# Kernel optimization log

Measured on AMD Instinct MI355X. Metric: run time of the kernel, lower is better.

The kernel has to match this reference:

```python
import jax, jax.numpy as jnp
import numpy as np

B, S, D, R = 8, 512, 768, 128


def setup_inputs() -> dict:
    key = jax.random.key(0)
    k1, k2, k3 = jax.random.split(key, 3)
    embeddings = jax.random.normal(k1, (B, S, D), dtype=jnp.float32)
    # nn.init.uniform_(proj, -0.05, 0.05)
    proj_dist = jax.random.uniform(k2, (R, D), dtype=jnp.float32, minval=-0.05, maxval=0.05)
    proj_depth = jax.random.uniform(k3, (R, D), dtype=jnp.float32, minval=-0.05, maxval=0.05)
    return {"embeddings": embeddings, "proj_dist": proj_dist, "proj_depth": proj_depth}


def _distances(embeddings, proj):
    # (B,S,D) @ (D,R) -> (B,S,R)
    p = jnp.einsum('bsd,rd->bsr', embeddings, proj)
    # pairwise squared euclidean distances: sum_r (p_i - p_j)^2 -> (B,S,S)
    diff = p[:, :, None, :] - p[:, None, :, :]
    return jnp.sum(diff * diff, axis=-1)


def _depths(embeddings, proj):
    p = jnp.einsum('bsd,rd->bsr', embeddings, proj)
    return jnp.sum(p * p, axis=-1)  # (B,S)


def reference(embeddings, proj_dist, proj_depth):
    distances = _distances(embeddings, proj_dist)
    depths = _depths(embeddings, proj_depth)
    return (distances, depths)
```

## Files before the change

### kernel.cpp

```cpp
#include <hip/hip_runtime.h>

#define NB 8
#define NS 512
#define ND 768
#define NR 128
#define NM (NB * NS)
#define DIST_ELEMS ((size_t)NB * NS * NS)

typedef short bf16x8 __attribute__((ext_vector_type(8)));
typedef __bf16 bfv8  __attribute__((ext_vector_type(8)));
typedef float f32x4  __attribute__((ext_vector_type(4)));

__device__ __forceinline__ unsigned short f2bf(float f) {
  return __builtin_bit_cast(unsigned short, (__bf16)f);
}
__device__ __forceinline__ float bf2f(unsigned short h) {
  return __uint_as_float(((unsigned int)h) << 16);
}
__device__ __forceinline__ bf16x8 pack8(float4 lo, float4 hi) {
  bfv8 v;
  v[0] = (__bf16)lo.x; v[1] = (__bf16)lo.y;
  v[2] = (__bf16)lo.z; v[3] = (__bf16)lo.w;
  v[4] = (__bf16)hi.x; v[5] = (__bf16)hi.y;
  v[6] = (__bf16)hi.z; v[7] = (__bf16)hi.w;
  return __builtin_bit_cast(bf16x8, v);
}

constexpr int KT  = 128;
constexpr int SAS = 136;

__global__ __launch_bounds__(256) void proj_kernel(
    const float* __restrict__ emb,
    const float* __restrict__ projD,
    const float* __restrict__ projP,
    unsigned short* __restrict__ P,
    float* __restrict__ nP0, float* __restrict__ nP1,
    float* __restrict__ nD0, float* __restrict__ nD1)
{
  __shared__ unsigned short sA[2][32][SAS];
  __shared__ float sRed[4][32];

  const int tid = threadIdx.x;
  const int m0  = blockIdx.x * 32;
  const int ct  = blockIdx.y;
  const bool isP = (ct < 2);
  const float* proj = (isP ? projD : projP) + (size_t)((ct & 1) * 64) * ND;

  const int ar = tid >> 3, ao = tid & 7;
  const float* aPtr = emb + (size_t)(m0 + ar) * ND + ao * 8;

  const int lane = tid & 63;
  const int w    = tid >> 6;
  const int ln   = lane & 15;
  const int q    = lane >> 4;

  const float* bRow = proj + (size_t)(16 * w + ln) * ND + q * 8;

  float4 a0, a1, a2, a3;
  a0 = *(const float4*)(aPtr);      a1 = *(const float4*)(aPtr + 4);
  a2 = *(const float4*)(aPtr + 64); a3 = *(const float4*)(aPtr + 68);

  f32x4 acc[2] = {};

  *(bf16x8*)(&sA[0][ar][ao * 8])       = pack8(a0, a1);
  *(bf16x8*)(&sA[0][ar][(ao + 8) * 8]) = pack8(a2, a3);
  __syncthreads();

  int p = 0;
  for (int kt = 0; kt < ND; kt += KT) {
    const bool more = (kt + KT < ND);
    if (more) {
      const int o = kt + KT;
      a0 = *(const float4*)(aPtr + o);      a1 = *(const float4*)(aPtr + o + 4);
      a2 = *(const float4*)(aPtr + o + 64); a3 = *(const float4*)(aPtr + o + 68);
    }
    bf16x8 bq[4];
    #pragma unroll
    for (int ks = 0; ks < 4; ++ks) {
      const float* bp = bRow + kt + ks * 32;
      float4 lo = *(const float4*)bp;
      float4 hi = *(const float4*)(bp + 4);
      bq[ks] = pack8(lo, hi);
    }
    #pragma unroll
    for (int ks = 0; ks < 4; ++ks) {
      #pragma unroll
      for (int i = 0; i < 2; ++i) {
        bf16x8 aq = *(const bf16x8*)(&sA[p][16 * i + ln][ks * 32 + q * 8]);
        acc[i] = __builtin_amdgcn_mfma_f32_16x16x32_bf16(aq, bq[ks], acc[i], 0, 0, 0);
      }
    }
    if (more) {
      *(bf16x8*)(&sA[p ^ 1][ar][ao * 8])       = pack8(a0, a1);
      *(bf16x8*)(&sA[p ^ 1][ar][(ao + 8) * 8]) = pack8(a2, a3);
    }
    __syncthreads();
    p ^= 1;
  }

  const int colG = (ct & 1) * 64 + 16 * w + ln;
  #pragma unroll
  for (int i = 0; i < 2; ++i)
    #pragma unroll
    for (int r = 0; r < 4; ++r) {
      unsigned short hb = f2bf(acc[i][r]);
      if (isP) P[(size_t)(m0 + 16 * i + 4 * q + r) * NR + colG] = hb;
      float v = bf2f(hb);
      float s = v * v;
      s += __shfl_xor(s, 1);
      s += __shfl_xor(s, 2);
      s += __shfl_xor(s, 4);
      s += __shfl_xor(s, 8);
      if (ln == 0) sRed[w][16 * i + 4 * q + r] = s;
    }
  __syncthreads();
  if (tid < 32) {
    float* np = (ct == 0) ? nP0 : (ct == 1) ? nP1 : (ct == 2) ? nD0 : nD1;
    np[m0 + tid] = sRed[0][tid] + sRed[1][tid] + sRed[2][tid] + sRed[3][tid];
  }
}

__global__ __launch_bounds__(256) void dist_kernel(
    const unsigned short* __restrict__ P,
    const float* __restrict__ nP0, const float* __restrict__ nP1,
    const float* __restrict__ nD0, const float* __restrict__ nD1,
    float* __restrict__ out,
    float* __restrict__ depths)
{
  __shared__ float nIs[64], nJs[64];

  const int tid = threadIdx.x;
  const int b  = blockIdx.z;
  const int i0 = blockIdx.y * 64;
  const int j0 = blockIdx.x * 64;
  const unsigned short* Pb = P + (size_t)b * NS * NR;
  const int mB = b * NS;

  if (tid < 64) {
    nIs[tid] = nP0[mB + i0 + tid] + nP1[mB + i0 + tid];
  } else if (tid < 128) {
    const int t = tid - 64;
    nJs[t] = nP0[mB + j0 + t] + nP1[mB + j0 + t];
  } else if (blockIdx.x == 0 && tid < 192) {
    const int t = tid - 128;
    depths[mB + i0 + t] = nD0[mB + i0 + t] + nD1[mB + i0 + t];
  }

  const int lane = tid & 63;
  const int w    = tid >> 6;
  const int ln   = lane & 15;
  const int q    = lane >> 4;

  bf16x8 aq[4][4], bq[4];
  #pragma unroll
  for (int ks = 0; ks < 4; ++ks) {
    bq[ks] = *(const bf16x8*)(Pb + (size_t)(j0 + 16 * w + ln) * NR + ks * 32 + q * 8);
    #pragma unroll
    for (int i = 0; i < 4; ++i)
      aq[i][ks] = *(const bf16x8*)(Pb + (size_t)(i0 + 16 * i + ln) * NR + ks * 32 + q * 8);
  }

  f32x4 acc[4] = {};
  #pragma unroll
  for (int ks = 0; ks < 4; ++ks)
    #pragma unroll
    for (int i = 0; i < 4; ++i)
      acc[i] = __builtin_amdgcn_mfma_f32_16x16x32_bf16(aq[i][ks], bq[ks], acc[i], 0, 0, 0);

  __syncthreads();

  const int col = j0 + 16 * w + ln;
  const float nj = nJs[16 * w + ln];
  float* ob = out + (size_t)b * NS * NS;
  #pragma unroll
  for (int i = 0; i < 4; ++i)
    #pragma unroll
    for (int r = 0; r < 4; ++r) {
      const int rloc = 16 * i + 4 * q + r;
      ob[(size_t)(i0 + rloc) * NS + col] = nIs[rloc] + nj - 2.0f * acc[i][r];
    }
}

extern "C" void kernel_launch(void* const* d_in, const int* in_sizes, int n_in,
                              void* d_out, int out_size, void* d_ws, size_t ws_size,
                              hipStream_t stream) {
  const float* emb   = (const float*)d_in[0];
  const float* projD = (const float*)d_in[1];
  const float* projP = (const float*)d_in[2];
  float* out = (float*)d_out;

  unsigned short* P = (unsigned short*)d_ws;
  float* nP0 = (float*)((char*)d_ws + (size_t)NM * NR * 2);
  float* nP1 = nP0 + NM;
  float* nD0 = nP1 + NM;
  float* nD1 = nD0 + NM;
  float* depths = out + DIST_ELEMS;

  proj_kernel<<<dim3(NM / 32, 4), 256, 0, stream>>>(emb, projD, projP, P, nP0, nP1, nD0, nD1);
  dist_kernel<<<dim3(NS / 64, NS / 64, NB), 256, 0, stream>>>(P, nP0, nP1, nD0, nD1, out, depths);
}
```

Baseline: 85.48 us.

## Register-prefetch next K-tile of A and B in proj kernel with single barrier

```diff
diff --git a/kernel.cpp b/kernel.cpp
--- a/kernel.cpp
+++ b/kernel.cpp
@@ -27,6 +27,7 @@
 }
 
 constexpr int KT  = 128;
+constexpr int NKT = ND / KT;
 constexpr int SAS = 136;
 
 __global__ __launch_bounds__(256) void proj_kernel(
@@ -56,46 +57,52 @@
 
   const float* bRow = proj + (size_t)(16 * w + ln) * ND + q * 8;
 
-  float4 a0, a1, a2, a3;
-  a0 = *(const float4*)(aPtr);      a1 = *(const float4*)(aPtr + 4);
-  a2 = *(const float4*)(aPtr + 64); a3 = *(const float4*)(aPtr + 68);
+  float4 Ar[2][4], Br[2][8];
+  Ar[0][0] = *(const float4*)(aPtr);      Ar[0][1] = *(const float4*)(aPtr + 4);
+  Ar[0][2] = *(const float4*)(aPtr + 64); Ar[0][3] = *(const float4*)(aPtr + 68);
+  Br[0][0] = *(const float4*)(bRow);      Br[0][1] = *(const float4*)(bRow + 4);
+  Br[0][2] = *(const float4*)(bRow + 32); Br[0][3] = *(const float4*)(bRow + 36);
+  Br[0][4] = *(const float4*)(bRow + 64); Br[0][5] = *(const float4*)(bRow + 68);
+  Br[0][6] = *(const float4*)(bRow + 96); Br[0][7] = *(const float4*)(bRow + 100);
 
   f32x4 acc[2] = {};
 
-  *(bf16x8*)(&sA[0][ar][ao * 8])       = pack8(a0, a1);
-  *(bf16x8*)(&sA[0][ar][(ao + 8) * 8]) = pack8(a2, a3);
-  __syncthreads();
-
-  int p = 0;
-  for (int kt = 0; kt < ND; kt += KT) {
-    const bool more = (kt + KT < ND);
-    if (more) {
-      const int o = kt + KT;
-      a0 = *(const float4*)(aPtr + o);      a1 = *(const float4*)(aPtr + o + 4);
-      a2 = *(const float4*)(aPtr + o + 64); a3 = *(const float4*)(aPtr + o + 68);
+  #pragma unroll
+  for (int t = 0; t < NKT; ++t) {
+    const int cur = t & 1;
+    *(bf16x8*)(&sA[cur][ar][ao * 8])       = pack8(Ar[cur][0], Ar[cur][1]);
+    *(bf16x8*)(&sA[cur][ar][(ao + 8) * 8]) = pack8(Ar[cur][2], Ar[cur][3]);
+    asm volatile("s_waitcnt lgkmcnt(0)" ::: "memory");
+    __builtin_amdgcn_s_barrier();
+    __builtin_amdgcn_sched_barrier(0);
+    if (t + 1 < NKT) {
+      const int o = (t + 1) * KT;
+      const int nxt = cur ^ 1;
+      Ar[nxt][0] = *(const float4*)(aPtr + o);
+      Ar[nxt][1] = *(const float4*)(aPtr + o + 4);
+      Ar[nxt][2] = *(const float4*)(aPtr + o + 64);
+      Ar[nxt][3] = *(const float4*)(aPtr + o + 68);
+      Br[nxt][0] = *(const float4*)(bRow + o);
+      Br[nxt][1] = *(const float4*)(bRow + o + 4);
+      Br[nxt][2] = *(const float4*)(bRow + o + 32);
+      Br[nxt][3] = *(const float4*)(bRow + o + 36);
+      Br[nxt][4] = *(const float4*)(bRow + o + 64);
+      Br[nxt][5] = *(const float4*)(bRow + o + 68);
+      Br[nxt][6] = *(const float4*)(bRow + o + 96);
+      Br[nxt][7] = *(const float4*)(bRow + o + 100);
     }
     bf16x8 bq[4];
     #pragma unroll
-    for (int ks = 0; ks < 4; ++ks) {
-      const float* bp = bRow + kt + ks * 32;
-      float4 lo = *(const float4*)bp;
-      float4 hi = *(const float4*)(bp + 4);
-      bq[ks] = pack8(lo, hi);
-    }
+    for (int ks = 0; ks < 4; ++ks)
+      bq[ks] = pack8(Br[cur][2 * ks], Br[cur][2 * ks + 1]);
     #pragma unroll
     for (int ks = 0; ks < 4; ++ks) {
       #pragma unroll
       for (int i = 0; i < 2; ++i) {
-        bf16x8 aq = *(const bf16x8*)(&sA[p][16 * i + ln][ks * 32 + q * 8]);
+        bf16x8 aq = *(const bf16x8*)(&sA[cur][16 * i + ln][ks * 32 + q * 8]);
         acc[i] = __builtin_amdgcn_mfma_f32_16x16x32_bf16(aq, bq[ks], acc[i], 0, 0, 0);
       }
     }
-    if (more) {
-      *(bf16x8*)(&sA[p ^ 1][ar][ao * 8])       = pack8(a0, a1);
-      *(bf16x8*)(&sA[p ^ 1][ar][(ao + 8) * 8]) = pack8(a2, a3);
-    }
-    __syncthreads();
-    p ^= 1;
   }
 
   const int colG = (ct & 1) * 64 + 16 * w + ln;
```

Measured after the change: 84.86 us. No clear change (-0.7%).
